# Optimization experiments

Hardware: AMD Instinct MI355X
Metric: run time of the kernel (lower is better)

Reference implementation:

```python
import jax, jax.numpy as jnp
import numpy as np

DIM = 256
NUM_HEADS = 8
KERNEL_SIZES = [7, 7]
DILATIONS = [1, 2]
NUM_SPLITS = 2
HEAD_DIM = DIM // NUM_HEADS
SCALE = HEAD_DIM ** -0.5


def _window_start(L, K, D):
    """NATTEN get_window_start, vectorized over indices 0..L-1 (static numpy)."""
    idx = np.arange(L)
    NH = K // 2
    if D <= 1:
        return np.maximum(idx - NH, 0) + (idx + NH >= L) * (L - idx - NH - 1)
    ni = idx - NH * D
    imodd = idx % D
    a = (L // D) * D
    b = L - a
    edge = np.where(imodd < b, L - b + imodd - 2 * NH * D, a + imodd - K * D)
    return np.where(ni < 0, imodd, np.where(idx + NH * D >= L, edge, ni))


def _pb_start(L, K, D):
    """NATTEN get_pb_start (relative position bias offset), static numpy."""
    idx = np.arange(L)
    NH = K // 2
    if D <= 1:
        return NH + (idx < NH) * (NH - idx) + (idx + NH >= L) * (L - idx - 1 - NH)
    return np.where(idx - NH * D < 0, K - 1 - idx // D,
                    np.where(idx + NH * D >= L, (L - idx - 1) // D, NH))


def _natten2d(q, k, v, rpb, K, D):
    # q,k,v: [B,h,H,W,d]; rpb: [h, 2K-1, 2K-1]
    B, h, H, W, d = q.shape
    ki = _window_start(H, K, D)[:, None] + D * np.arange(K)   # [H,K]
    kj = _window_start(W, K, D)[:, None] + D * np.arange(K)   # [W,K]
    bi = _pb_start(H, K, D)[:, None] + np.arange(K)           # [H,K]
    bj = _pb_start(W, K, D)[:, None] + np.arange(K)           # [W,K]
    kg = jnp.take(jnp.take(k, ki, axis=2), kj, axis=4)        # [B,h,H,K,W,K,d]
    vg = jnp.take(jnp.take(v, ki, axis=2), kj, axis=4)        # [B,h,H,K,W,K,d]
    attn = jnp.einsum('bhijd,bhiujvd->bhijuv', q, kg)         # [B,h,H,W,K,K]
    bias = jnp.take(jnp.take(rpb, bi, axis=1), bj, axis=3)    # [h,H,K,W,K]
    attn = attn + bias.transpose(0, 1, 3, 2, 4)[None]
    attn = jax.nn.softmax(attn.reshape(B, h, H, W, K * K), axis=-1)
    attn = attn.reshape(B, h, H, W, K, K)
    return jnp.einsum('bhijuv,bhiujvd->bhijd', attn, vg)      # [B,h,H,W,d]


def setup_inputs() -> dict:
    key = jax.random.key(0)
    ks = jax.random.split(key, 6)
    B, C, H, W = 2, DIM, 56, 56
    x = jax.random.normal(ks[0], (B, C, H, W), dtype=jnp.float32)
    w_qkv1 = jax.random.normal(ks[1], (3 * C, C), dtype=jnp.float32) * (C ** -0.5)
    w_qkv2 = jax.random.normal(ks[2], (3 * C, 1, 3, 3), dtype=jnp.float32) * (1.0 / 3.0)
    rpb0 = jax.random.truncated_normal(ks[3], -2.0, 2.0,
                                       (NUM_HEADS // NUM_SPLITS, 13, 13), dtype=jnp.float32) * 0.02
    rpb1 = jax.random.truncated_normal(ks[4], -2.0, 2.0,
                                       (NUM_HEADS // NUM_SPLITS, 13, 13), dtype=jnp.float32) * 0.02
    w_proj = jax.random.normal(ks[5], (C, C), dtype=jnp.float32) * (C ** -0.5)
    return {"x": x, "w_qkv1": w_qkv1, "w_qkv2": w_qkv2,
            "rpb0": rpb0, "rpb1": rpb1, "w_proj": w_proj}


def reference(x, w_qkv1, w_qkv2, rpb0, rpb1, w_proj):
    B, C, H, W = x.shape
    # qkv: 1x1 conv (no bias) then depthwise 3x3 conv (no bias)
    y = jnp.einsum('oc,bchw->bohw', w_qkv1, x)
    y = jax.lax.conv_general_dilated(
        y, w_qkv2, window_strides=(1, 1), padding='SAME',
        dimension_numbers=('NCHW', 'OIHW', 'NCHW'), feature_group_count=3 * C)
    # Faithful to torch: raw reshape of [B,3C,H,W] -> [B,H,W,3,nh,hd]
    qkv = y.reshape(B, H, W, 3, NUM_HEADS, HEAD_DIM).transpose(3, 0, 4, 1, 2, 5)
    q, k, v = qkv[0] * SCALE, qkv[1], qkv[2]   # [B,nh,H,W,hd]
    hs = NUM_HEADS // NUM_SPLITS
    rpbs = [rpb0, rpb1]
    outs = []
    for s in range(NUM_SPLITS):
        sl = slice(s * hs, (s + 1) * hs)
        outs.append(_natten2d(q[:, sl], k[:, sl], v[:, sl],
                              rpbs[s], KERNEL_SIZES[s], DILATIONS[s]))
    o = jnp.concatenate(outs, axis=1)                 # [B,nh,H,W,hd]
    o = o.transpose(0, 1, 4, 2, 3).reshape(B, C, H, W)
    return jnp.einsum('oc,bchw->bohw', w_proj, o)
```

## Files before the change

### kernel.cpp

```cpp
#include <hip/hip_runtime.h>
#include <hip/hip_bf16.h>

#define HGT 56
#define WID 56
#define SPA 3136
#define CCH 256
#define C3  768
#define NH  8
#define HD  32
#define YB  2408448
#define ISTR 43008
#define JSTR 768
#define SCALE_Q 0.17677669529663687f

typedef __attribute__((ext_vector_type(8))) short short8;
typedef __attribute__((ext_vector_type(4))) float f32x4;

static __device__ __forceinline__ unsigned short f2bf_bits(float f) {
    __hip_bfloat16 h = __float2bfloat16(f);
    union { __hip_bfloat16 h; unsigned short u; } cv; cv.h = h; return cv.u;
}
static __device__ __forceinline__ float bf_lo(unsigned u) {
    union { unsigned x; float f; } c; c.x = u << 16; return c.f;
}
static __device__ __forceinline__ float bf_hi(unsigned u) {
    union { unsigned x; float f; } c; c.x = u & 0xffff0000u; return c.f;
}

__global__ __launch_bounds__(256) void k_cvt(const float* __restrict__ x,
                                             const float* __restrict__ w1,
                                             const float* __restrict__ wp,
                                             __hip_bfloat16* __restrict__ xT,
                                             __hip_bfloat16* __restrict__ w1b,
                                             __hip_bfloat16* __restrict__ wpb) {
    __shared__ __align__(16) __hip_bfloat16 Sl[64][80];
    const int t = threadIdx.x;
    const int z = blockIdx.z;
    if (z == 2) {
        const int gid = (blockIdx.y * 49 + blockIdx.x) * 256 + t;
        for (int i = gid * 4; i < 262144; i += 200704) {
            const float* src;
            __hip_bfloat16* dst;
            if (i < 196608) { src = w1 + i; dst = w1b + i; }
            else            { src = wp + (i - 196608); dst = wpb + (i - 196608); }
            float4 v = *(const float4*)src;
            ushort4 u;
            u.x = f2bf_bits(v.x); u.y = f2bf_bits(v.y);
            u.z = f2bf_bits(v.z); u.w = f2bf_bits(v.w);
            *(ushort4*)dst = u;
        }
        return;
    }
    const int b = z, c0 = blockIdx.y * 64, s0 = blockIdx.x * 64;
    const float* xb = x + (size_t)b * (CCH * SPA);
    const int sq = (t & 15) * 4, cq = (t >> 4) * 4;
    float4 r[4];
#pragma unroll
    for (int rr = 0; rr < 4; ++rr)
        r[rr] = *(const float4*)&xb[(size_t)(c0 + cq + rr) * SPA + s0 + sq];
#pragma unroll
    for (int j = 0; j < 4; ++j) {
        ushort4 u;
        u.x = f2bf_bits(((const float*)&r[0])[j]);
        u.y = f2bf_bits(((const float*)&r[1])[j]);
        u.z = f2bf_bits(((const float*)&r[2])[j]);
        u.w = f2bf_bits(((const float*)&r[3])[j]);
        *(ushort4*)&Sl[sq + j][cq] = u;
    }
    __syncthreads();
    const int srow = t >> 2, cslot = t & 3;
    __hip_bfloat16* dst = &xT[(size_t)b * SPA * CCH + (size_t)(s0 + srow) * CCH + c0];
    short8 v0 = *(const short8*)&Sl[srow][cslot * 8];
    short8 v1 = *(const short8*)&Sl[srow][(cslot + 4) * 8];
    *(short8*)&dst[cslot * 8] = v0;
    *(short8*)&dst[(cslot + 4) * 8] = v1;
}

__global__ __launch_bounds__(256) void k_gemm(const __hip_bfloat16* __restrict__ A,
                                              const __hip_bfloat16* __restrict__ B,
                                              float* __restrict__ C, int M) {
    __shared__ __align__(16) short sA[4096];
    __shared__ __align__(16) short sB[4096];
    const int t = threadIdx.x;
    const int lane = t & 63, w = t >> 6;
    const int s0 = blockIdx.x * 64, o0 = blockIdx.y * 64, b = blockIdx.z;
    const __hip_bfloat16* Bb = B + (size_t)b * SPA * CCH;

    const int srow = t >> 3;
    const int scol = (t & 7) ^ (srow & 7);
    const char* gA = (const char*)(A  + (size_t)(o0 + srow) * CCH) + scol * 16;
    const char* gB = (const char*)(Bb + (size_t)(s0 + srow) * CCH) + scol * 16;
    char* lA = (char*)sA + w * 1024;
    char* lB = (char*)sB + w * 1024;

    const int wm = w >> 1, wn = w & 1;
    const int lr = lane & 15, kh = lane >> 4;
    const int ar0 = wm * 32 + lr, ar1 = ar0 + 16;
    const int br0 = wn * 32 + lr, br1 = br0 + 16;

    f32x4 acc[2][2] = {};
    for (int kt = 0; kt < 4; ++kt) {
        __builtin_amdgcn_global_load_lds(
            (const __attribute__((address_space(1))) void*)(gA + kt * 128),
            (__attribute__((address_space(3))) void*)lA, 16, 0, 0);
        __builtin_amdgcn_global_load_lds(
            (const __attribute__((address_space(1))) void*)(gA + 16384 + kt * 128),
            (__attribute__((address_space(3))) void*)(lA + 4096), 16, 0, 0);
        __builtin_amdgcn_global_load_lds(
            (const __attribute__((address_space(1))) void*)(gB + kt * 128),
            (__attribute__((address_space(3))) void*)lB, 16, 0, 0);
        __builtin_amdgcn_global_load_lds(
            (const __attribute__((address_space(1))) void*)(gB + 16384 + kt * 128),
            (__attribute__((address_space(3))) void*)(lB + 4096), 16, 0, 0);
        __syncthreads();
#pragma unroll
        for (int kk = 0; kk < 2; ++kk) {
            const int kg = (kk << 2) | kh;
            short8 a0 = *(const short8*)&sA[(ar0 * 128 + ((kg ^ (ar0 & 7)) << 4)) >> 1];
            short8 a1 = *(const short8*)&sA[(ar1 * 128 + ((kg ^ (ar1 & 7)) << 4)) >> 1];
            short8 b0 = *(const short8*)&sB[(br0 * 128 + ((kg ^ (br0 & 7)) << 4)) >> 1];
            short8 b1 = *(const short8*)&sB[(br1 * 128 + ((kg ^ (br1 & 7)) << 4)) >> 1];
            acc[0][0] = __builtin_amdgcn_mfma_f32_16x16x32_bf16(a0, b0, acc[0][0], 0, 0, 0);
            acc[0][1] = __builtin_amdgcn_mfma_f32_16x16x32_bf16(a0, b1, acc[0][1], 0, 0, 0);
            acc[1][0] = __builtin_amdgcn_mfma_f32_16x16x32_bf16(a1, b0, acc[1][0], 0, 0, 0);
            acc[1][1] = __builtin_amdgcn_mfma_f32_16x16x32_bf16(a1, b1, acc[1][1], 0, 0, 0);
        }
        __syncthreads();
    }
    float* Cb = C + (size_t)b * M * SPA;
#pragma unroll
    for (int mi = 0; mi < 2; ++mi)
#pragma unroll
        for (int ni = 0; ni < 2; ++ni) {
            const int r0 = o0 + wm * 32 + mi * 16 + kh * 4;
            const int cc = s0 + wn * 32 + ni * 16 + lr;
#pragma unroll
            for (int q = 0; q < 4; ++q)
                Cb[(size_t)(r0 + q) * SPA + cc] = acc[mi][ni][q];
        }
}

__global__ __launch_bounds__(256) void k_dw(const float* __restrict__ y1,
                                            const float* __restrict__ w2,
                                            __hip_bfloat16* __restrict__ y2) {
    int idx = blockIdx.x * 256 + threadIdx.x;
    int tw = idx % 14;
    int rest = idx / 14;
    int h = rest % HGT;
    int bc = rest / HGT;
    int w0 = tw * 4;
    const float* in = y1 + (size_t)bc * SPA;
    const float* wt = w2 + (bc % C3) * 9;
    float4 acc = {0.f, 0.f, 0.f, 0.f};
#pragma unroll
    for (int dh = -1; dh <= 1; ++dh) {
        int hh = h + dh;
        if (hh < 0 || hh >= HGT) continue;
        const float* rp = in + hh * WID + w0;
        float4 c = *(const float4*)rp;
        float l = (w0 > 0) ? rp[-1] : 0.f;
        float r = (w0 < 52) ? rp[4] : 0.f;
        float wl = wt[(dh + 1) * 3 + 0];
        float wc = wt[(dh + 1) * 3 + 1];
        float wr = wt[(dh + 1) * 3 + 2];
        acc.x += wl * l   + wc * c.x + wr * c.y;
        acc.y += wl * c.x + wc * c.y + wr * c.z;
        acc.z += wl * c.y + wc * c.z + wr * c.w;
        acc.w += wl * c.z + wc * c.w + wr * r;
    }
    ushort4 o;
    o.x = f2bf_bits(acc.x); o.y = f2bf_bits(acc.y);
    o.z = f2bf_bits(acc.z); o.w = f2bf_bits(acc.w);
    *(ushort4*)(y2 + (size_t)bc * SPA + h * WID + w0) = o;
}

template<int D>
__device__ __forceinline__ void attn_body(short* __restrict__ Kl,
                                          short* __restrict__ Vl,
                                          float* __restrict__ biasl,
                                          int* __restrict__ cpvt,
                                          const __hip_bfloat16* __restrict__ y2,
                                          const float* __restrict__ rpb,
                                          __hip_bfloat16* __restrict__ opre,
                                          int b, int head, int i, int half_, int hsub) {
    const int tid = threadIdx.x;
    const int lane = tid & 63, wid = tid >> 6;
    const int cmin = half_ ? 21 : 0;

    int wsi, pbi;
    if (D == 1) {
        wsi = (i < 3) ? 0 : ((i > 52) ? 49 : i - 3);
        pbi = (i < 3) ? 6 - i : ((i > 52) ? 55 - i : 3);
    } else {
        wsi = (i < 6) ? (i & 1) : ((i >= 50) ? 42 + (i & 1) : i - 6);
        pbi = (i < 6) ? 6 - (i >> 1) : ((i >= 50) ? (55 - i) >> 1 : 3);
    }

    const __hip_bfloat16* ybase = y2 + (size_t)b * YB + head * HD;

    const __hip_bfloat16* kbase = ybase + CCH     + wsi * ISTR + cmin * JSTR;
    const __hip_bfloat16* vbase = ybase + 2 * CCH + wsi * ISTR + cmin * JSTR;
    for (int f = tid; f < 1960; f += 256) {
        const bool isV = f >= 980;
        const int g = isV ? f - 980 : f;
        const int col = g / 28;
        const int rem = g - col * 28;
        const int u = rem >> 2, r = rem & 3;
        const __hip_bfloat16* src = (isV ? vbase : kbase) + u * (D * ISTR) + col * JSTR + r * 8;
        short8 s = *(const short8*)src;
        const int colS = (!isV && D == 2) ? ((col >> 1) + (col & 1) * 18) : col;
        short* dst = isV ? Vl : Kl;
        *(short8*)&dst[(colS * 7 + u) * 40 + r * 8] = s;
    }
    if (tid < 169) biasl[tid] = rpb[hsub * 169 + tid];
    if (tid < 52) {
        int uu = tid / 7, vv = tid - uu * 7;
        cpvt[tid] = (tid < 49) ? (D * vv * 7 + uu) * 20 : 0;
    }
    __syncthreads();

    int u = lane / 7, v = lane - u * 7;
    const bool act = lane < 49;
    if (!act) { u = 0; v = 0; }
    const int bconst = u * 13 + v + pbi * 13;
    const int qt = lane >> 4, dp = lane & 15;
    const unsigned* Vw = (const unsigned*)Vl;

    int cpw[13];
#pragma unroll
    for (int t = 0; t < 13; ++t) cpw[t] = cpvt[qt * 13 + t];

    const int j0 = half_ * 28 + wid * 7;

    float qA[32], qB[32];
#define LOADQ(dst, jx)                                                        \
    {                                                                         \
        const short8* qp = (const short8*)(ybase + i * ISTR + (jx) * JSTR);   \
        _Pragma("unroll")                                                     \
        for (int r = 0; r < 4; ++r) {                                         \
            short8 tq = qp[r];                                                \
            const unsigned* tu = (const unsigned*)&tq;                        \
            _Pragma("unroll")                                                 \
            for (int e = 0; e < 4; ++e) {                                     \
                dst[8 * r + 2 * e]     = bf_lo(tu[e]);                        \
                dst[8 * r + 2 * e + 1] = bf_hi(tu[e]);                        \
            }                                                                 \
        }                                                                     \
    }

    auto body = [&](const float (&q)[32], float (&qn)[32], int jj, bool pre) {
        const int j = j0 + jj;
        int wsj, pbj;
        if (D == 1) {
            wsj = (j < 3) ? 0 : ((j > 52) ? 49 : j - 3);
            pbj = (j < 3) ? 6 - j : ((j > 52) ? 55 - j : 3);
        } else {
            wsj = (j < 6) ? (j & 1) : ((j >= 50) ? 42 + (j & 1) : j - 6);
            pbj = (j < 6) ? 6 - (j >> 1) : ((j >= 50) ? (55 - j) >> 1 : 3);
        }
        if (pre) LOADQ(qn, j + 1);
        const int kcol0 = wsj - cmin;

        int rrl;
        if (D == 1) rrl = (kcol0 + v) * 7 + u;
        else {
            const int kc = kcol0 + 2 * v;
            rrl = ((kc >> 1) + (kc & 1) * 18) * 7 + u;
        }
        const short* kp = &Kl[rrl * 40];
        float acc = 0.f;
#pragma unroll
        for (int s = 0; s < 4; ++s) {
            short8 kk = *(const short8*)(kp + s * 8);
            const unsigned* ku = (const unsigned*)&kk;
#pragma unroll
            for (int e = 0; e < 4; ++e) {
                acc += q[s * 8 + 2 * e]     * bf_lo(ku[e]);
                acc += q[s * 8 + 2 * e + 1] * bf_hi(ku[e]);
            }
        }

        float e = act ? __expf(acc * SCALE_Q + biasl[bconst + pbj]) : 0.f;
        float ssum = e;
#pragma unroll
        for (int off = 32; off; off >>= 1) ssum += __shfl_xor(ssum, off);
        const float wgt = e * __frcp_rn(ssum);

        const int vbw = kcol0 * 140 + dp;
        float o0 = 0.f, o1 = 0.f;
#pragma unroll
        for (int t = 0; t < 13; ++t) {
            const float wv = __shfl(wgt, qt * 13 + t);
            const unsigned vw = Vw[vbw + cpw[t]];
            o0 += wv * bf_lo(vw);
            o1 += wv * bf_hi(vw);
        }
        o0 += __shfl_xor(o0, 16); o0 += __shfl_xor(o0, 32);
        o1 += __shfl_xor(o1, 16); o1 += __shfl_xor(o1, 32);
        if (lane < 16) {
            union { ushort2 s; unsigned w; } pk;
            pk.s.x = f2bf_bits(o0);
            pk.s.y = f2bf_bits(o1);
            *(unsigned*)&opre[(size_t)b * (SPA * CCH) +
                              (size_t)(i * WID + j) * CCH + head * HD + dp * 2] = pk.w;
        }
    };

    LOADQ(qA, j0);
    body(qA, qB, 0, true);
    body(qB, qA, 1, true);
    body(qA, qB, 2, true);
    body(qB, qA, 3, true);
    body(qA, qB, 4, true);
    body(qB, qA, 5, true);
    body(qA, qB, 6, false);
#undef LOADQ
}

__global__ __launch_bounds__(256) void k_attn5(const __hip_bfloat16* __restrict__ y2,
                                               const float* __restrict__ rpb0,
                                               const float* __restrict__ rpb1,
                                               __hip_bfloat16* __restrict__ opre) {
    __shared__ __align__(16) short Kl[9800];
    __shared__ __align__(16) short Vl[9800];
    __shared__ float biasl[169];
    __shared__ int   cpvt[52];
    const int half_ = blockIdx.x;
    const int i = blockIdx.y;
    const int bh = blockIdx.z;
    const int b = bh >> 3, head = bh & 7;
    if (head < 4)
        attn_body<1>(Kl, Vl, biasl, cpvt, y2, rpb0, opre, b, head, i, half_, head);
    else
        attn_body<2>(Kl, Vl, biasl, cpvt, y2, rpb1, opre, b, head, i, half_, head - 4);
}

extern "C" void kernel_launch(void* const* d_in, const int* in_sizes, int n_in,
                              void* d_out, int out_size, void* d_ws, size_t ws_size,
                              hipStream_t stream) {
    const float* x    = (const float*)d_in[0];
    const float* w1   = (const float*)d_in[1];
    const float* w2   = (const float*)d_in[2];
    const float* rpb0 = (const float*)d_in[3];
    const float* rpb1 = (const float*)d_in[4];
    const float* wp   = (const float*)d_in[5];
    float* out = (float*)d_out;

    float* p = (float*)d_ws;
    float* y1 = p;
    __hip_bfloat16* y2b  = (__hip_bfloat16*)(p + 2 * YB);
    __hip_bfloat16* xT   = (__hip_bfloat16*)(p + 3 * YB);
    __hip_bfloat16* opre = xT;
    __hip_bfloat16* w1b  = (__hip_bfloat16*)(p + 3 * YB + 802816);
    __hip_bfloat16* wpb  = (__hip_bfloat16*)(p + 3 * YB + 802816 + 98304);

    k_cvt<<<dim3(49, 4, 3), 256, 0, stream>>>(x, w1, wp, xT, w1b, wpb);
    k_gemm<<<dim3(49, 12, 2), 256, 0, stream>>>(w1b, xT, y1, C3);
    k_dw<<<dim3(4704), 256, 0, stream>>>(y1, w2, y2b);
    k_attn5<<<dim3(2, HGT, 2 * NH), 256, 0, stream>>>(y2b, rpb0, rpb1, opre);
    k_gemm<<<dim3(49, 4, 2), 256, 0, stream>>>(wpb, opre, out, CCH);
}
```

Baseline: 66.09 us.

## Store qkv GEMM output as bf16 and software-pipeline attention softmax phases

The first GEMM now writes its intermediate in bf16 instead of fp32, and the depthwise conv reads bf16. This halves the intermediate traffic between the two kernels but adds one more rounding step. The attention inner loop is split into two phases, QK/exp and PV/normalize, and interleaved across consecutive columns to overlap latency. It also defers the softmax normalization until after the PV accumulation and splits the dot-product accumulator in two to shorten the dependency chain.

```diff
diff --git a/kernel.cpp b/kernel.cpp
--- a/kernel.cpp
+++ b/kernel.cpp
@@ -25,6 +25,9 @@
 }
 static __device__ __forceinline__ float bf_hi(unsigned u) {
     union { unsigned x; float f; } c; c.x = u & 0xffff0000u; return c.f;
+}
+static __device__ __forceinline__ float bfu(unsigned short u) {
+    union { unsigned x; float f; } c; c.x = (unsigned)u << 16; return c.f;
 }
 
 __global__ __launch_bounds__(256) void k_cvt(const float* __restrict__ x,
@@ -76,9 +79,10 @@
     *(short8*)&dst[(cslot + 4) * 8] = v1;
 }
 
+template<bool OBF>
 __global__ __launch_bounds__(256) void k_gemm(const __hip_bfloat16* __restrict__ A,
                                               const __hip_bfloat16* __restrict__ B,
-                                              float* __restrict__ C, int M) {
+                                              void* __restrict__ Cv, int M) {
     __shared__ __align__(16) short sA[4096];
     __shared__ __align__(16) short sB[4096];
     const int t = threadIdx.x;
@@ -127,20 +131,27 @@
         }
         __syncthreads();
     }
-    float* Cb = C + (size_t)b * M * SPA;
 #pragma unroll
     for (int mi = 0; mi < 2; ++mi)
 #pragma unroll
         for (int ni = 0; ni < 2; ++ni) {
             const int r0 = o0 + wm * 32 + mi * 16 + kh * 4;
             const int cc = s0 + wn * 32 + ni * 16 + lr;
-#pragma unroll
-            for (int q = 0; q < 4; ++q)
-                Cb[(size_t)(r0 + q) * SPA + cc] = acc[mi][ni][q];
-        }
-}
-
-__global__ __launch_bounds__(256) void k_dw(const float* __restrict__ y1,
+            if constexpr (OBF) {
+                __hip_bfloat16* Cb = (__hip_bfloat16*)Cv + (size_t)b * M * SPA;
+#pragma unroll
+                for (int q = 0; q < 4; ++q)
+                    Cb[(size_t)(r0 + q) * SPA + cc] = __float2bfloat16(acc[mi][ni][q]);
+            } else {
+                float* Cb = (float*)Cv + (size_t)b * M * SPA;
+#pragma unroll
+                for (int q = 0; q < 4; ++q)
+                    Cb[(size_t)(r0 + q) * SPA + cc] = acc[mi][ni][q];
+            }
+        }
+}
+
+__global__ __launch_bounds__(256) void k_dw(const __hip_bfloat16* __restrict__ y1,
                                             const float* __restrict__ w2,
                                             __hip_bfloat16* __restrict__ y2) {
     int idx = blockIdx.x * 256 + threadIdx.x;
@@ -149,28 +160,29 @@
     int h = rest % HGT;
     int bc = rest / HGT;
     int w0 = tw * 4;
-    const float* in = y1 + (size_t)bc * SPA;
+    const __hip_bfloat16* in = y1 + (size_t)bc * SPA;
     const float* wt = w2 + (bc % C3) * 9;
-    float4 acc = {0.f, 0.f, 0.f, 0.f};
+    float a0 = 0.f, a1 = 0.f, a2 = 0.f, a3 = 0.f;
 #pragma unroll
     for (int dh = -1; dh <= 1; ++dh) {
         int hh = h + dh;
         if (hh < 0 || hh >= HGT) continue;
-        const float* rp = in + hh * WID + w0;
-        float4 c = *(const float4*)rp;
-        float l = (w0 > 0) ? rp[-1] : 0.f;
-        float r = (w0 < 52) ? rp[4] : 0.f;
+        const __hip_bfloat16* rp = in + hh * WID + w0;
+        ushort4 c4 = *(const ushort4*)rp;
+        float c0 = bfu(c4.x), c1 = bfu(c4.y), c2 = bfu(c4.z), c3 = bfu(c4.w);
+        float l = (w0 > 0)  ? bfu(*(const unsigned short*)(rp - 1)) : 0.f;
+        float r = (w0 < 52) ? bfu(*(const unsigned short*)(rp + 4)) : 0.f;
         float wl = wt[(dh + 1) * 3 + 0];
         float wc = wt[(dh + 1) * 3 + 1];
         float wr = wt[(dh + 1) * 3 + 2];
-        acc.x += wl * l   + wc * c.x + wr * c.y;
-        acc.y += wl * c.x + wc * c.y + wr * c.z;
-        acc.z += wl * c.y + wc * c.z + wr * c.w;
-        acc.w += wl * c.z + wc * c.w + wr * r;
+        a0 += wl * l  + wc * c0 + wr * c1;
+        a1 += wl * c0 + wc * c1 + wr * c2;
+        a2 += wl * c1 + wc * c2 + wr * c3;
+        a3 += wl * c2 + wc * c3 + wr * r;
     }
     ushort4 o;
-    o.x = f2bf_bits(acc.x); o.y = f2bf_bits(acc.y);
-    o.z = f2bf_bits(acc.z); o.w = f2bf_bits(acc.w);
+    o.x = f2bf_bits(a0); o.y = f2bf_bits(a1);
+    o.z = f2bf_bits(a2); o.w = f2bf_bits(a3);
     *(ushort4*)(y2 + (size_t)bc * SPA + h * WID + w0) = o;
 }
 
@@ -231,25 +243,27 @@
     for (int t = 0; t < 13; ++t) cpw[t] = cpvt[qt * 13 + t];
 
     const int j0 = half_ * 28 + wid * 7;
+    const size_t obase = (size_t)b * (SPA * CCH) + (size_t)(i * WID) * CCH + head * HD + dp * 2;
 
     float qA[32], qB[32];
-#define LOADQ(dst, jx)                                                        \
-    {                                                                         \
-        const short8* qp = (const short8*)(ybase + i * ISTR + (jx) * JSTR);   \
-        _Pragma("unroll")                                                     \
-        for (int r = 0; r < 4; ++r) {                                         \
-            short8 tq = qp[r];                                                \
-            const unsigned* tu = (const unsigned*)&tq;                        \
-            _Pragma("unroll")                                                 \
-            for (int e = 0; e < 4; ++e) {                                     \
-                dst[8 * r + 2 * e]     = bf_lo(tu[e]);                        \
-                dst[8 * r + 2 * e + 1] = bf_hi(tu[e]);                        \
-            }                                                                 \
-        }                                                                     \
-    }
-
-    auto body = [&](const float (&q)[32], float (&qn)[32], int jj, bool pre) {
-        const int j = j0 + jj;
+    float eA, eB;
+    int kA, kB;
+
+    auto loadq = [&](float (&dst)[32], int jx) {
+        const short8* qp = (const short8*)(ybase + i * ISTR + jx * JSTR);
+#pragma unroll
+        for (int r = 0; r < 4; ++r) {
+            short8 tq = qp[r];
+            const unsigned* tu = (const unsigned*)&tq;
+#pragma unroll
+            for (int e = 0; e < 4; ++e) {
+                dst[8 * r + 2 * e]     = bf_lo(tu[e]);
+                dst[8 * r + 2 * e + 1] = bf_hi(tu[e]);
+            }
+        }
+    };
+
+    auto phase1 = [&](const float (&q)[32], int j, float& eo, int& ko) {
         int wsj, pbj;
         if (D == 1) {
             wsj = (j < 3) ? 0 : ((j > 52) ? 49 : j - 3);
@@ -258,9 +272,8 @@
             wsj = (j < 6) ? (j & 1) : ((j >= 50) ? 42 + (j & 1) : j - 6);
             pbj = (j < 6) ? 6 - (j >> 1) : ((j >= 50) ? (55 - j) >> 1 : 3);
         }
-        if (pre) LOADQ(qn, j + 1);
         const int kcol0 = wsj - cmin;
-
+        ko = kcol0;
         int rrl;
         if (D == 1) rrl = (kcol0 + v) * 7 + u;
         else {
@@ -268,56 +281,56 @@
             rrl = ((kc >> 1) + (kc & 1) * 18) * 7 + u;
         }
         const short* kp = &Kl[rrl * 40];
-        float acc = 0.f;
+        float a0 = 0.f, a1 = 0.f;
 #pragma unroll
         for (int s = 0; s < 4; ++s) {
             short8 kk = *(const short8*)(kp + s * 8);
             const unsigned* ku = (const unsigned*)&kk;
+            float& ac = (s < 2) ? a0 : a1;
 #pragma unroll
             for (int e = 0; e < 4; ++e) {
-                acc += q[s * 8 + 2 * e]     * bf_lo(ku[e]);
-                acc += q[s * 8 + 2 * e + 1] * bf_hi(ku[e]);
+                ac += q[s * 8 + 2 * e]     * bf_lo(ku[e]);
+                ac += q[s * 8 + 2 * e + 1] * bf_hi(ku[e]);
             }
         }
-
-        float e = act ? __expf(acc * SCALE_Q + biasl[bconst + pbj]) : 0.f;
-        float ssum = e;
-#pragma unroll
-        for (int off = 32; off; off >>= 1) ssum += __shfl_xor(ssum, off);
-        const float wgt = e * __frcp_rn(ssum);
-
-        const int vbw = kcol0 * 140 + dp;
+        eo = act ? __expf((a0 + a1) * SCALE_Q + biasl[bconst + pbj]) : 0.f;
+    };
+
+    auto phase2 = [&](float ev, int kc, int jx) {
+        const int vbw = kc * 140 + dp;
         float o0 = 0.f, o1 = 0.f;
 #pragma unroll
         for (int t = 0; t < 13; ++t) {
-            const float wv = __shfl(wgt, qt * 13 + t);
+            const float wv = __shfl(ev, qt * 13 + t);
             const unsigned vw = Vw[vbw + cpw[t]];
             o0 += wv * bf_lo(vw);
             o1 += wv * bf_hi(vw);
         }
+        float ssum = ev;
+#pragma unroll
+        for (int off = 32; off; off >>= 1) ssum += __shfl_xor(ssum, off);
         o0 += __shfl_xor(o0, 16); o0 += __shfl_xor(o0, 32);
         o1 += __shfl_xor(o1, 16); o1 += __shfl_xor(o1, 32);
+        const float rinv = __frcp_rn(ssum);
         if (lane < 16) {
             union { ushort2 s; unsigned w; } pk;
-            pk.s.x = f2bf_bits(o0);
-            pk.s.y = f2bf_bits(o1);
-            *(unsigned*)&opre[(size_t)b * (SPA * CCH) +
-                              (size_t)(i * WID + j) * CCH + head * HD + dp * 2] = pk.w;
+            pk.s.x = f2bf_bits(o0 * rinv);
+            pk.s.y = f2bf_bits(o1 * rinv);
+            *(unsigned*)&opre[obase + (size_t)jx * CCH] = pk.w;
         }
     };
 
-    LOADQ(qA, j0);
-    body(qA, qB, 0, true);
-    body(qB, qA, 1, true);
-    body(qA, qB, 2, true);
-    body(qB, qA, 3, true);
-    body(qA, qB, 4, true);
-    body(qB, qA, 5, true);
-    body(qA, qB, 6, false);
-#undef LOADQ
-}
-
-__global__ __launch_bounds__(256) void k_attn5(const __hip_bfloat16* __restrict__ y2,
+    loadq(qA, j0);          phase1(qA, j0,     eA, kA);
+    loadq(qB, j0 + 1);      phase1(qB, j0 + 1, eB, kB);  phase2(eA, kA, j0);
+    loadq(qA, j0 + 2);      phase1(qA, j0 + 2, eA, kA);  phase2(eB, kB, j0 + 1);
+    loadq(qB, j0 + 3);      phase1(qB, j0 + 3, eB, kB);  phase2(eA, kA, j0 + 2);
+    loadq(qA, j0 + 4);      phase1(qA, j0 + 4, eA, kA);  phase2(eB, kB, j0 + 3);
+    loadq(qB, j0 + 5);      phase1(qB, j0 + 5, eB, kB);  phase2(eA, kA, j0 + 4);
+    loadq(qA, j0 + 6);      phase1(qA, j0 + 6, eA, kA);  phase2(eB, kB, j0 + 5);
+    phase2(eA, kA, j0 + 6);
+}
+
+__global__ __launch_bounds__(256) void k_attn6(const __hip_bfloat16* __restrict__ y2,
                                                const float* __restrict__ rpb0,
                                                const float* __restrict__ rpb1,
                                                __hip_bfloat16* __restrict__ opre) {
@@ -347,16 +360,16 @@
     float* out = (float*)d_out;
 
     float* p = (float*)d_ws;
-    float* y1 = p;
-    __hip_bfloat16* y2b  = (__hip_bfloat16*)(p + 2 * YB);
-    __hip_bfloat16* xT   = (__hip_bfloat16*)(p + 3 * YB);
+    __hip_bfloat16* y1b  = (__hip_bfloat16*)p;
+    __hip_bfloat16* y2b  = (__hip_bfloat16*)(p + YB);
+    __hip_bfloat16* xT   = (__hip_bfloat16*)(p + 2 * YB);
     __hip_bfloat16* opre = xT;
-    __hip_bfloat16* w1b  = (__hip_bfloat16*)(p + 3 * YB + 802816);
-    __hip_bfloat16* wpb  = (__hip_bfloat16*)(p + 3 * YB + 802816 + 98304);
+    __hip_bfloat16* w1b  = (__hip_bfloat16*)(p + 2 * YB + 802816);
+    __hip_bfloat16* wpb  = (__hip_bfloat16*)(p + 2 * YB + 802816 + 98304);
 
     k_cvt<<<dim3(49, 4, 3), 256, 0, stream>>>(x, w1, wp, xT, w1b, wpb);
-    k_gemm<<<dim3(49, 12, 2), 256, 0, stream>>>(w1b, xT, y1, C3);
-    k_dw<<<dim3(4704), 256, 0, stream>>>(y1, w2, y2b);
-    k_attn5<<<dim3(2, HGT, 2 * NH), 256, 0, stream>>>(y2b, rpb0, rpb1, opre);
-    k_gemm<<<dim3(49, 4, 2), 256, 0, stream>>>(wpb, opre, out, CCH);
-}
+    k_gemm<true><<<dim3(49, 12, 2), 256, 0, stream>>>(w1b, xT, (void*)y1b, C3);
+    k_dw<<<dim3(4704), 256, 0, stream>>>(y1b, w2, y2b);
+    k_attn6<<<dim3(2, HGT, 2 * NH), 256, 0, stream>>>(y2b, rpb0, rpb1, opre);
+    k_gemm<false><<<dim3(49, 4, 2), 256, 0, stream>>>(wpb, opre, (void*)out, CCH);
+}
```

Result: faster. 63.85 us (-3.4%).
